# Performance work log

Hardware: AMD Instinct MI355X
Metric: run time of the kernel (lower is better)

The kernel has to match this reference:

```python
import jax, jax.numpy as jnp
import numpy as np

SOM_H, SOM_W = 16, 16
K = SOM_H * SOM_W          # num_embeddings = 256
EMB_D = 32                 # embedding_dim
ALPHA, BETA = 6.0, 1.0


def _build_tables():
    """Static SOM grid neighbor tables (rectangular geometry).
    ind[k] is a 0/1 row over the K codebook entries marking k and its
    up/down/left/right grid neighbors; counts[k] = number of neighbors incl self.
    Replaces the original per-voxel Python loop with a constant lookup table.
    """
    ind = np.zeros((K, K), np.float32)
    for idx in range(K):
        h, w = divmod(idx, SOM_W)
        neigh = [idx]
        if h - 1 >= 0:
            neigh.append((h - 1) * SOM_W + w)
        if h + 1 < SOM_H:
            neigh.append((h + 1) * SOM_W + w)
        if w - 1 >= 0:
            neigh.append(h * SOM_W + (w - 1))
        if w + 1 < SOM_W:
            neigh.append(h * SOM_W + (w + 1))
        ind[idx, neigh] = 1.0
    counts = ind.sum(axis=1)
    return jnp.asarray(ind), jnp.asarray(counts)

_IND_TABLE, _COUNTS = _build_tables()


def setup_inputs() -> dict:
    key = jax.random.key(0)
    k1, k2 = jax.random.split(key)
    x = jax.random.normal(k1, (8, EMB_D, 32, 32, 32), dtype=jnp.float32)  # [B,C,D,H,W]
    W = jax.random.normal(k2, (K, EMB_D), dtype=jnp.float32)              # codebook
    return {"x": x, "W": W}


def reference(x, W):
    # channels-last: [B, D, H, Wd, C]
    inputs = jnp.transpose(x, (0, 2, 3, 4, 1))
    in_shape = inputs.shape
    flat = inputs.reshape(-1, EMB_D)                    # [N, d]
    flat_sg = jax.lax.stop_gradient(flat)               # matches flat_inputs.detach()

    # squared Euclidean distances to all codebook entries: [N, K]
    dist = (jnp.sum(flat_sg ** 2, axis=1, keepdims=True)
            + jnp.sum(W ** 2, axis=1)
            - 2.0 * flat_sg @ W.T)

    enc_idx = jnp.argmin(dist, axis=1)                  # [N]
    encodings = jax.nn.one_hot(enc_idx, K, dtype=inputs.dtype)  # [N, K]

    quantized = (encodings @ W).reshape(in_shape)
    commitment_loss = jnp.mean((quantized - inputs) ** 2)

    # vectorized neighbor indicator + counts via static table gather
    indicator = _IND_TABLE[enc_idx]                     # [N, K], constant wrt floats
    total_neighbors = jnp.sum(_COUNTS[enc_idx])
    somloss = jnp.sum(dist * indicator) / total_neighbors

    loss = ALPHA * commitment_loss + BETA * somloss

    # straight-through estimator
    quantized_st = inputs + jax.lax.stop_gradient(quantized - inputs)
    out = jnp.transpose(quantized_st, (0, 4, 1, 2, 3))  # back to [B,C,D,H,W]
    return loss, out, encodings
```

## Files before the change

### kernel.cpp

```cpp
#include <hip/hip_runtime.h>


#define SOM_K      256
#define EMB_D      32
#define WPAD       36
#define N_VOX      262144
#define SPATIAL    32768
#define OUT_ELEMS  8388608
#define COMMIT_DEN 8388608.0f
#define NSLOT      256

#define CONST_AS __attribute__((address_space(4)))

__global__ __launch_bounds__(256) void som_prep_kernel(float* __restrict__ ws) {
  float4* p = (float4*)ws;
  int t = threadIdx.x;
#pragma unroll
  for (int i = 0; i < 4; ++i) p[i * 256 + t] = make_float4(0.f, 0.f, 0.f, 0.f);
}

__global__ __launch_bounds__(256, 4) void som_main_kernel(
    const float* __restrict__ x,
    const float* __restrict__ w,
    float* __restrict__ slots,
    float* __restrict__ out,
    float* __restrict__ enc) {
  __shared__ __align__(16) float wl[SOM_K * WPAD];
  __shared__ float wsql[SOM_K];

  const int t = threadIdx.x;
  const CONST_AS float* wcp = (const CONST_AS float*)(unsigned long long)w;

  const int n    = blockIdx.x * 256 + t;
  const int base = (n >> 15) * (EMB_D * SPATIAL) + (n & (SPATIAL - 1));
  float xv[EMB_D];
#pragma unroll
  for (int c = 0; c < EMB_D; ++c) xv[c] = x[base + c * SPATIAL];

#pragma unroll
  for (int i = 0; i < 32; ++i) {
    int e = i * 256 + t;
    int r = e >> 5, c = e & 31;
    wl[r * WPAD + c] = w[e];
  }
  __syncthreads();

  {
    const float4* row = (const float4*)(wl + t * WPAD);
    float s = 0.0f;
#pragma unroll
    for (int j = 0; j < 8; ++j) {
      float4 q = row[j];
      s = fmaf(q.x, q.x, s);
      s = fmaf(q.y, q.y, s);
      s = fmaf(q.z, q.z, s);
      s = fmaf(q.w, q.w, s);
    }
    wsql[t] = s;
  }

  float xsq = 0.0f;
#pragma unroll
  for (int c = 0; c < EMB_D; ++c) xsq = fmaf(xv[c], xv[c], xsq);
  __syncthreads();

  {
    const int lane = t & 63, wave = t >> 6;
    float* rb = enc + (size_t)(blockIdx.x * 256 + wave * 64) * SOM_K;
    float4* rb4 = (float4*)(rb + 3);
    const float4 z4 = make_float4(0.f, 0.f, 0.f, 0.f);
    for (int r = 0; r < 63; ++r) rb4[r * 64 + lane] = z4;
    if (lane < 63) rb4[4032 + lane] = z4;
    if (lane == 0)       { rb[0] = 0.f; rb[1] = 0.f; rb[2] = 0.f; }
    else if (lane == 63) { rb[16383] = 0.f; }
  }

  float best = 3.402823466e38f;
  int   bidx = 0;
#pragma unroll 2
  for (int k = 0; k < SOM_K; ++k) {
    const CONST_AS float* wr = wcp + (k << 5);
    float dot = 0.0f;
#pragma unroll
    for (int j = 0; j < EMB_D; ++j) dot = fmaf(wr[j], xv[j], dot);
    float d = (xsq + wsql[k]) - 2.0f * dot;
    if (d < best) { best = d; bidx = k; }
  }

  asm volatile("s_waitcnt vmcnt(0)" ::: "memory");
  enc[(size_t)n * SOM_K + bidx] = 1.0f;

  float commit = 0.0f;
  {
    const float4* qrow = (const float4*)(wl + bidx * WPAD);
#pragma unroll
    for (int j = 0; j < 8; ++j) {
      float4 q = qrow[j];
      float qq[4] = { q.x, q.y, q.z, q.w };
#pragma unroll
      for (int u = 0; u < 4; ++u) {
        int c = 4 * j + u;
        out[base + c * SPATIAL] = qq[u];
        float df = qq[u] - xv[c];
        commit = fmaf(df, df, commit);
      }
    }
  }

  float som = best;
  float cnt = 1.0f;
  {
    const int h   = bidx >> 4;
    const int wc2 = bidx & 15;
    const int   cand[4]  = { bidx - 16, bidx + 16, bidx - 1, bidx + 1 };
    const float valid[4] = { h > 0 ? 1.f : 0.f,  h < 15 ? 1.f : 0.f,
                             wc2 > 0 ? 1.f : 0.f, wc2 < 15 ? 1.f : 0.f };
#pragma unroll
    for (int j = 0; j < 4; ++j) {
      int nk = valid[j] != 0.0f ? cand[j] : bidx;
      const float4* nrow = (const float4*)(wl + nk * WPAD);
      float dot = 0.0f;
#pragma unroll
      for (int jj = 0; jj < 8; ++jj) {
        float4 q = nrow[jj];
        dot = fmaf(q.x, xv[4 * jj + 0], dot);
        dot = fmaf(q.y, xv[4 * jj + 1], dot);
        dot = fmaf(q.z, xv[4 * jj + 2], dot);
        dot = fmaf(q.w, xv[4 * jj + 3], dot);
      }
      float d = (xsq + wsql[nk]) - 2.0f * dot;
      som = fmaf(valid[j], d, som);
      cnt += valid[j];
    }
  }

  for (int off = 32; off > 0; off >>= 1) {
    commit += __shfl_down(commit, off, 64);
    som    += __shfl_down(som,    off, 64);
    cnt    += __shfl_down(cnt,    off, 64);
  }
  if ((t & 63) == 0) {
    float* sp = slots + (size_t)(blockIdx.x & (NSLOT - 1)) * 16;
    atomicAdd(sp + 0, commit);
    atomicAdd(sp + 1, som);
    atomicAdd(sp + 2, cnt);
  }
}

__global__ __launch_bounds__(64) void som_final_kernel(
    const float* __restrict__ slots, float* __restrict__ loss) {
  const int t = threadIdx.x;
  float commit = 0.f, som = 0.f, cnt = 0.f;
#pragma unroll
  for (int i = 0; i < 4; ++i) {
    const float* sp = slots + (size_t)(i * 64 + t) * 16;
    commit += sp[0]; som += sp[1]; cnt += sp[2];
  }
  for (int off = 32; off > 0; off >>= 1) {
    commit += __shfl_down(commit, off, 64);
    som    += __shfl_down(som,    off, 64);
    cnt    += __shfl_down(cnt,    off, 64);
  }
  if (t == 0) loss[0] = 6.0f * (commit / COMMIT_DEN) + som / cnt;
}

extern "C" void kernel_launch(void* const* d_in, const int* in_sizes, int n_in,
                              void* d_out, int out_size, void* d_ws, size_t ws_size,
                              hipStream_t stream) {
  const float* x = (const float*)d_in[0];
  const float* w = (const float*)d_in[1];
  float* ws  = (float*)d_ws;
  float* o   = (float*)d_out;

  som_prep_kernel<<<1, 256, 0, stream>>>(ws);
  som_main_kernel<<<N_VOX / 256, 256, 0, stream>>>(
      x, w, ws, o + 1, o + 1 + OUT_ELEMS);
  som_final_kernel<<<1, 64, 0, stream>>>(ws, o);
}
```

Measured before the change: 406.3 us.

## Split codebook search across two wave halves with shared-memory argmin merge

```diff
diff --git a/kernel.cpp b/kernel.cpp
--- a/kernel.cpp
+++ b/kernel.cpp
@@ -19,33 +19,40 @@
   for (int i = 0; i < 4; ++i) p[i * 256 + t] = make_float4(0.f, 0.f, 0.f, 0.f);
 }
 
-__global__ __launch_bounds__(256, 4) void som_main_kernel(
+__global__ __launch_bounds__(512, 6) void som_main_kernel(
     const float* __restrict__ x,
     const float* __restrict__ w,
     float* __restrict__ slots,
     float* __restrict__ out,
     float* __restrict__ enc) {
   __shared__ __align__(16) float wl[SOM_K * WPAD];
-  __shared__ float wsql[SOM_K];
-
-  const int t = threadIdx.x;
+  __shared__ __align__(16) float wsql[SOM_K];
+  __shared__ float sbest[256];
+  __shared__ int   sbidx[256];
+
+  const int t    = threadIdx.x;
+  const int lane = t & 63;
+  const int wave = __builtin_amdgcn_readfirstlane(t >> 6);
+  const int half = wave >> 2;
+  const int vloc = ((wave & 3) << 6) + lane;
+  const int n    = blockIdx.x * 256 + vloc;
+  const int base = (n >> 15) * (EMB_D * SPATIAL) + (n & (SPATIAL - 1));
+
   const CONST_AS float* wcp = (const CONST_AS float*)(unsigned long long)w;
 
-  const int n    = blockIdx.x * 256 + t;
-  const int base = (n >> 15) * (EMB_D * SPATIAL) + (n & (SPATIAL - 1));
   float xv[EMB_D];
 #pragma unroll
   for (int c = 0; c < EMB_D; ++c) xv[c] = x[base + c * SPATIAL];
 
 #pragma unroll
-  for (int i = 0; i < 32; ++i) {
-    int e = i * 256 + t;
+  for (int i = 0; i < 16; ++i) {
+    int e = i * 512 + t;
     int r = e >> 5, c = e & 31;
     wl[r * WPAD + c] = w[e];
   }
   __syncthreads();
 
-  {
+  if (t < SOM_K) {
     const float4* row = (const float4*)(wl + t * WPAD);
     float s = 0.0f;
 #pragma unroll
@@ -65,29 +72,47 @@
   __syncthreads();
 
   {
-    const int lane = t & 63, wave = t >> 6;
-    float* rb = enc + (size_t)(blockIdx.x * 256 + wave * 64) * SOM_K;
+    float* rb = enc + (size_t)(blockIdx.x * 256 + wave * 32) * SOM_K;
     float4* rb4 = (float4*)(rb + 3);
     const float4 z4 = make_float4(0.f, 0.f, 0.f, 0.f);
-    for (int r = 0; r < 63; ++r) rb4[r * 64 + lane] = z4;
-    if (lane < 63) rb4[4032 + lane] = z4;
+    for (int r = 0; r < 32; ++r) {
+      int idx = r * 64 + lane;
+      if (idx < 2047) rb4[idx] = z4;
+    }
     if (lane == 0)       { rb[0] = 0.f; rb[1] = 0.f; rb[2] = 0.f; }
-    else if (lane == 63) { rb[16383] = 0.f; }
-  }
-
+    else if (lane == 63) { rb[8191] = 0.f; }
+  }
+
+  const int klo = half << 7;
   float best = 3.402823466e38f;
-  int   bidx = 0;
-#pragma unroll 2
-  for (int k = 0; k < SOM_K; ++k) {
-    const CONST_AS float* wr = wcp + (k << 5);
-    float dot = 0.0f;
-#pragma unroll
-    for (int j = 0; j < EMB_D; ++j) dot = fmaf(wr[j], xv[j], dot);
-    float d = (xsq + wsql[k]) - 2.0f * dot;
-    if (d < best) { best = d; bidx = k; }
-  }
-
-  asm volatile("s_waitcnt vmcnt(0)" ::: "memory");
+  int   bidx = klo;
+#pragma unroll 1
+  for (int k2 = 0; k2 < 128; k2 += 2) {
+    const CONST_AS float* r0 = wcp + ((klo + k2) << 5);
+    const CONST_AS float* r1 = r0 + 32;
+    float d0 = 0.0f, d1 = 0.0f;
+#pragma unroll
+    for (int j = 0; j < EMB_D; ++j) {
+      const float xj = xv[j];
+      d0 = fmaf(r0[j], xj, d0);
+      d1 = fmaf(r1[j], xj, d1);
+    }
+    const float e0 = (xsq + wsql[klo + k2])     - 2.0f * d0;
+    const float e1 = (xsq + wsql[klo + k2 + 1]) - 2.0f * d1;
+    if (e0 < best) { best = e0; bidx = klo + k2;     }
+    if (e1 < best) { best = e1; bidx = klo + k2 + 1; }
+  }
+
+  if (half == 1) { sbest[vloc] = best; sbidx[vloc] = bidx; }
+  __syncthreads();
+  if (half == 1) return;
+
+  {
+    const float s1 = sbest[vloc];
+    const int   k1 = sbidx[vloc];
+    if (s1 < best) { best = s1; bidx = k1; }
+  }
+
   enc[(size_t)n * SOM_K + bidx] = 1.0f;
 
   float commit = 0.0f;
@@ -139,7 +164,7 @@
     som    += __shfl_down(som,    off, 64);
     cnt    += __shfl_down(cnt,    off, 64);
   }
-  if ((t & 63) == 0) {
+  if (lane == 0) {
     float* sp = slots + (size_t)(blockIdx.x & (NSLOT - 1)) * 16;
     atomicAdd(sp + 0, commit);
     atomicAdd(sp + 1, som);
@@ -173,7 +198,7 @@
   float* o   = (float*)d_out;
 
   som_prep_kernel<<<1, 256, 0, stream>>>(ws);
-  som_main_kernel<<<N_VOX / 256, 256, 0, stream>>>(
+  som_main_kernel<<<N_VOX / 256, 512, 0, stream>>>(
       x, w, ws, o + 1, o + 1 + OUT_ELEMS);
   som_final_kernel<<<1, 64, 0, stream>>>(ws, o);
 }
```

New measurement: 426.3 us. +4.9%, slower.
